# Kernel tuning notes

Measured on AMD Instinct MI355X. Metric: run time of the kernel, lower is better.

The kernel has to match this reference:

```python
import jax, jax.numpy as jnp
import numpy as np

N_NODES = 100000
N_EDGES = 1600000
IN_FEATS = 64
OUT_FEATS = 64
EDGE_FEATS = 1


def setup_inputs() -> dict:
    key = jax.random.key(0)
    ks = jax.random.split(key, 6)
    h = jax.random.normal(ks[0], (N_NODES, IN_FEATS), dtype=jnp.float32)
    e = jax.random.normal(ks[1], (N_EDGES, EDGE_FEATS), dtype=jnp.float32)
    src = jax.random.randint(ks[2], (N_EDGES,), 0, N_NODES, dtype=jnp.int32)
    dst = jax.random.randint(ks[3], (N_EDGES,), 0, N_NODES, dtype=jnp.int32)
    cat_dim = 2 * IN_FEATS + EDGE_FEATS  # 129
    W1 = jax.random.normal(ks[4], (cat_dim, OUT_FEATS), dtype=jnp.float32) / np.sqrt(cat_dim)
    b1 = jnp.zeros((OUT_FEATS,), dtype=jnp.float32)
    W2 = jax.random.normal(ks[5], (OUT_FEATS, OUT_FEATS), dtype=jnp.float32) / np.sqrt(OUT_FEATS)
    b2 = jnp.zeros((OUT_FEATS,), dtype=jnp.float32)
    return {"h": h, "e": e, "src": src, "dst": dst, "W1": W1, "b1": b1, "W2": W2, "b2": b2}


def reference(h, e, src, dst, W1, b1, W2, b2):
    # Gather per-edge features: [src_h | dst_h | e] -> (E, 2*in+edge_dim)
    x = jnp.concatenate([h[src], h[dst], e], axis=1)
    # Two-layer MLP on edges
    m = jax.nn.relu(x @ W1 + b1) @ W2 + b2  # (E, out_feats)
    # Scatter-sum messages to destination nodes
    h_new = jax.ops.segment_sum(m, dst, num_segments=h.shape[0])  # (N, out_feats)
    return h_new
```

## Files before the change

kernel.cpp:

```cpp
#include <hip/hip_runtime.h>
#include <hip/hip_bf16.h>


#define PRE_NPB 128

typedef unsigned int u32;

__device__ __forceinline__ void gload_lds16(const float* g, float* l) {
    __builtin_amdgcn_global_load_lds(
        (const __attribute__((address_space(1))) u32*)g,
        (__attribute__((address_space(3))) u32*)l,
        16, 0, 0);
}

__global__ __launch_bounds__(256) void alloc_offs_kernel(const int* __restrict__ counts,
                                                         int* __restrict__ gcursor,
                                                         int* __restrict__ offs, int n) {
    __shared__ int wsum[4];
    const int i    = blockIdx.x * 256 + threadIdx.x;
    const int lane = threadIdx.x & 63;
    const int wv   = threadIdx.x >> 6;

    const int c = (i < n) ? counts[i] : 0;
    int incl = c;
    #pragma unroll
    for (int d = 1; d < 64; d <<= 1) {
        int v = __shfl_up(incl, d, 64);
        if (lane >= d) incl += v;
    }
    const int excl = incl - c;
    if (lane == 63) wsum[wv] = incl;
    __syncthreads();
    if (threadIdx.x == 0) {
        const int s0 = wsum[0], s1 = wsum[1], s2 = wsum[2], s3 = wsum[3];
        const int b = atomicAdd(gcursor, s0 + s1 + s2 + s3);
        wsum[0] = b; wsum[1] = b + s0; wsum[2] = b + s0 + s1; wsum[3] = b + s0 + s1 + s2;
    }
    __syncthreads();
    if (i < n) offs[i] = wsum[wv] + excl;
}

__global__ void fill_kernel(const int* __restrict__ dst, const int* __restrict__ src,
                            const float* __restrict__ e,
                            const int* __restrict__ offs, const int* __restrict__ rank,
                            int2* __restrict__ meta, int n_edges) {
    const int i = blockIdx.x * blockDim.x + threadIdx.x;
    if (i >= n_edges) return;
    const int d = dst[i];
    meta[offs[d] + rank[i]] = make_int2(src[i], __float_as_int(e[i]));
}

__global__ __launch_bounds__(256, 2) void pre_count_kernel(
    const float* __restrict__ h, const float* __restrict__ W1, const float* __restrict__ b1,
    unsigned short* __restrict__ abf, unsigned short* __restrict__ bsf, int n_nodes,
    const int* __restrict__ dst, int* __restrict__ counts, int* __restrict__ rank,
    int n_edges, int pg)
{
    __shared__ float hbuf[2][64 * 64];
    const int lane = threadIdx.x & 63;
    const int wv   = threadIdx.x >> 6;

    if ((int)blockIdx.x >= pg) {
        const int i = ((int)blockIdx.x - pg) * 256 + threadIdx.x;
        if (i < n_edges) rank[i] = atomicAdd(&counts[dst[i]], 1);
        return;
    }

    const int base = blockIdx.x * PRE_NPB;
    if (base >= n_nodes) return;
    const int nrem   = n_nodes - base;
    const int ntiles = (nrem >= PRE_NPB) ? (PRE_NPB / 64) : ((nrem + 63) >> 6);

    float wreg[128];
    #pragma unroll
    for (int k = 0; k < 128; ++k) wreg[k] = W1[(size_t)k * 64 + lane];
    #pragma unroll
    for (int k = 0; k < 128; ++k) asm volatile("" : "+v"(wreg[k]));
    const float b1l = b1[lane];

    auto stage = [&](int buf, int node_base) {
        if (node_base + 64 <= n_nodes) {
            const float* gsrc = h + (size_t)node_base * 64;
            #pragma unroll
            for (int q = 0; q < 4; ++q) {
                const int c = wv * 4 + q;
                gload_lds16(gsrc + c * 256 + lane * 4, &hbuf[buf][c * 256]);
            }
        } else {
            #pragma unroll
            for (int q = 0; q < 4; ++q) {
                const int f4 = threadIdx.x + 256 * q;
                const long gf = (long)node_base * 16 + f4;
                float4 v = make_float4(0.f, 0.f, 0.f, 0.f);
                if (gf < (long)n_nodes * 16)
                    v = reinterpret_cast<const float4*>(h)[gf];
                reinterpret_cast<float4*>(hbuf[buf])[f4] = v;
            }
        }
    };

    auto consume = [&](int buf, int node_base) {
        for (int i = 0; i < 16; ++i) {
            const int ln = wv * 16 + i;
            const int n  = node_base + ln;
            if (n < n_nodes) {
                const float4* hr = reinterpret_cast<const float4*>(&hbuf[buf][ln * 64]);
                float4 h4[16];
                #pragma unroll
                for (int k4 = 0; k4 < 16; ++k4) h4[k4] = hr[k4];
                float av = 0.f, bv = b1l;
                #pragma unroll
                for (int k4 = 0; k4 < 16; ++k4) {
                    av = fmaf(h4[k4].x, wreg[4 * k4 + 0], av);
                    bv = fmaf(h4[k4].x, wreg[64 + 4 * k4 + 0], bv);
                    av = fmaf(h4[k4].y, wreg[4 * k4 + 1], av);
                    bv = fmaf(h4[k4].y, wreg[64 + 4 * k4 + 1], bv);
                    av = fmaf(h4[k4].z, wreg[4 * k4 + 2], av);
                    bv = fmaf(h4[k4].z, wreg[64 + 4 * k4 + 2], bv);
                    av = fmaf(h4[k4].w, wreg[4 * k4 + 3], av);
                    bv = fmaf(h4[k4].w, wreg[64 + 4 * k4 + 3], bv);
                }
                __hip_bfloat16 ab = __float2bfloat16(av);
                __hip_bfloat16 bb = __float2bfloat16(bv);
                abf[(size_t)n * 64 + lane] = *reinterpret_cast<unsigned short*>(&ab);
                bsf[(size_t)n * 64 + lane] = *reinterpret_cast<unsigned short*>(&bb);
            }
        }
    };

    stage(0, base);
    __syncthreads();
    for (int t = 0; t < ntiles; ++t) {
        if (t + 1 < ntiles) stage((t + 1) & 1, base + (t + 1) * 64);
        consume(t & 1, base + t * 64);
        __syncthreads();
    }
}

__global__ __launch_bounds__(256) void node_accum_kernel(
    const unsigned short* __restrict__ abf, const unsigned short* __restrict__ bsf,
    const float* __restrict__ W1, const float* __restrict__ W2, const float* __restrict__ b2,
    const int* __restrict__ offs, const int* __restrict__ counts,
    const int2* __restrict__ meta, float* __restrict__ out, int n_nodes)
{
    const int lane = threadIdx.x & 63;
    const int wv   = __builtin_amdgcn_readfirstlane(threadIdx.x >> 6);
    const int n    = blockIdx.x * 4 + wv;
    if (n >= n_nodes) return;

    const float basel = __uint_as_float((uint)bsf[(size_t)n * 64 + lane] << 16);
    const float w128l = W1[(size_t)128 * 64 + lane];
    float acc = 0.f;

    const int beg = offs[n];
    const int np  = counts[n];

    for (int c0 = 0; c0 < np; c0 += 64) {
        const int cn = min(np - c0, 64);

        int mx = 0, my = 0;
        if (lane < cn) {
            const int2 m = meta[beg + c0 + lane];
            mx = m.x; my = m.y;
        }

        uint x0=0,x1=0,x2=0,x3=0,x4=0,x5=0,x6=0,x7=0;

        auto ld = [&](int j, uint& x) {
            const int s = __builtin_amdgcn_readlane(mx, j);
            x = (uint)abf[(size_t)s * 64 + lane];
        };
        auto step = [&](int j, uint xr) {
            const float ev = __uint_as_float((uint)__builtin_amdgcn_readlane(my, j));
            const float xv = __uint_as_float(xr << 16);
            acc += fmaxf(fmaf(ev, w128l, basel) + xv, 0.f);
        };

        if (cn > 0) ld(0, x0);
        if (cn > 1) ld(1, x1);
        if (cn > 2) ld(2, x2);
        if (cn > 3) ld(3, x3);
        if (cn > 4) ld(4, x4);
        if (cn > 5) ld(5, x5);
        if (cn > 6) ld(6, x6);
        if (cn > 7) ld(7, x7);

        int i = 0;
        while (i + 16 <= cn) {
            step(i + 0, x0); ld(i + 8,  x0);
            step(i + 1, x1); ld(i + 9,  x1);
            step(i + 2, x2); ld(i + 10, x2);
            step(i + 3, x3); ld(i + 11, x3);
            step(i + 4, x4); ld(i + 12, x4);
            step(i + 5, x5); ld(i + 13, x5);
            step(i + 6, x6); ld(i + 14, x6);
            step(i + 7, x7); ld(i + 15, x7);
            i += 8;
        }
        const int r = cn - i;
        if (r > 0)  { step(i + 0, x0); }  if (r > 8)  { ld(i + 8,  x0); }
        if (r > 1)  { step(i + 1, x1); }  if (r > 9)  { ld(i + 9,  x1); }
        if (r > 2)  { step(i + 2, x2); }  if (r > 10) { ld(i + 10, x2); }
        if (r > 3)  { step(i + 3, x3); }  if (r > 11) { ld(i + 11, x3); }
        if (r > 4)  { step(i + 4, x4); }  if (r > 12) { ld(i + 12, x4); }
        if (r > 5)  { step(i + 5, x5); }  if (r > 13) { ld(i + 13, x5); }
        if (r > 6)  { step(i + 6, x6); }  if (r > 14) { ld(i + 14, x6); }
        if (r > 7)  { step(i + 7, x7); }
        if (r > 8)  { step(i + 8,  x0); }
        if (r > 9)  { step(i + 9,  x1); }
        if (r > 10) { step(i + 10, x2); }
        if (r > 11) { step(i + 11, x3); }
        if (r > 12) { step(i + 12, x4); }
        if (r > 13) { step(i + 13, x5); }
        if (r > 14) { step(i + 14, x6); }
    }

    float o = (float)np * b2[lane];
    #pragma unroll
    for (int j = 0; j < 64; ++j) {
        const float aj = __shfl(acc, j, 64);
        o = fmaf(aj, W2[(size_t)j * 64 + lane], o);
    }
    out[(size_t)n * 64 + lane] = o;
}

extern "C" void kernel_launch(void* const* d_in, const int* in_sizes, int n_in,
                              void* d_out, int out_size, void* d_ws, size_t ws_size,
                              hipStream_t stream) {
    const float* h  = (const float*)d_in[0];
    const float* e  = (const float*)d_in[1];
    const int* src  = (const int*)d_in[2];
    const int* dst  = (const int*)d_in[3];
    const float* W1 = (const float*)d_in[4];
    const float* b1 = (const float*)d_in[5];
    const float* W2 = (const float*)d_in[6];
    const float* b2 = (const float*)d_in[7];
    float* out = (float*)d_out;

    const int n_edges = in_sizes[2];
    const int N = in_sizes[0] / 64;

    int* counts  = (int*)d_ws;
    int* gcursor = counts + N;
    int* offs    = gcursor + 8;
    int* rank    = offs + N;
    int2* meta   = (int2*)(rank + n_edges);
    unsigned short* abf = (unsigned short*)(meta + n_edges);
    unsigned short* bsf = abf + (size_t)64 * N;

    hipMemsetAsync(counts, 0, ((size_t)N + 8) * sizeof(int), stream);

    const int eb = (n_edges + 255) / 256;
    const int nb = (N + 255) / 256;
    const int pg = (N + PRE_NPB - 1) / PRE_NPB;

    pre_count_kernel<<<pg + eb, 256, 0, stream>>>(h, W1, b1, abf, bsf, N,
                                                  dst, counts, rank, n_edges, pg);
    alloc_offs_kernel<<<nb, 256, 0, stream>>>(counts, gcursor, offs, N);
    fill_kernel<<<eb, 256, 0, stream>>>(dst, src, e, offs, rank, meta, n_edges);
    node_accum_kernel<<<(N + 3) / 4, 256, 0, stream>>>(abf, bsf, W1, W2, b2,
                                                       offs, counts, meta, out, N);
}
```

Before: 202.0 us.

## Replace LDS-staged node projection with register-resident h and readlane broadcasts

```diff
diff --git a/kernel.cpp b/kernel.cpp
--- a/kernel.cpp
+++ b/kernel.cpp
@@ -5,13 +5,6 @@
 #define PRE_NPB 128
 
 typedef unsigned int u32;
-
-__device__ __forceinline__ void gload_lds16(const float* g, float* l) {
-    __builtin_amdgcn_global_load_lds(
-        (const __attribute__((address_space(1))) u32*)g,
-        (__attribute__((address_space(3))) u32*)l,
-        16, 0, 0);
-}
 
 __global__ __launch_bounds__(256) void alloc_offs_kernel(const int* __restrict__ counts,
                                                          int* __restrict__ gcursor,
@@ -56,7 +49,6 @@
     const int* __restrict__ dst, int* __restrict__ counts, int* __restrict__ rank,
     int n_edges, int pg)
 {
-    __shared__ float hbuf[2][64 * 64];
     const int lane = threadIdx.x & 63;
     const int wv   = threadIdx.x >> 6;
 
@@ -66,74 +58,88 @@
         return;
     }
 
-    const int base = blockIdx.x * PRE_NPB;
-    if (base >= n_nodes) return;
-    const int nrem   = n_nodes - base;
-    const int ntiles = (nrem >= PRE_NPB) ? (PRE_NPB / 64) : ((nrem + 63) >> 6);
-
-    float wreg[128];
-    #pragma unroll
-    for (int k = 0; k < 128; ++k) wreg[k] = W1[(size_t)k * 64 + lane];
-    #pragma unroll
-    for (int k = 0; k < 128; ++k) asm volatile("" : "+v"(wreg[k]));
-    const float b1l = b1[lane];
-
-    auto stage = [&](int buf, int node_base) {
-        if (node_base + 64 <= n_nodes) {
-            const float* gsrc = h + (size_t)node_base * 64;
+    const int nbase = (blockIdx.x * 4 + wv) * 32;
+    if (nbase >= n_nodes) return;
+
+    const float4* h4p = reinterpret_cast<const float4*>(h);
+
+    auto ldgrp = [&](int g) -> float4 {
+        float4 v = make_float4(0.f, 0.f, 0.f, 0.f);
+        const int row = nbase + 4 * g + (lane >> 4);
+        if (g < 8 && row < n_nodes)
+            v = h4p[(size_t)(nbase + 4 * g) * 16 + lane];
+        return v;
+    };
+
+    {
+        float wreg[64];
+        #pragma unroll
+        for (int k = 0; k < 64; ++k) wreg[k] = W1[(size_t)k * 64 + lane];
+        #pragma unroll
+        for (int k = 0; k < 64; ++k) asm volatile("" : "+v"(wreg[k]));
+
+        float4 cur = ldgrp(0);
+        for (int g = 0; g < 8; ++g) {
+            const float4 nxt = ldgrp(g + 1);
             #pragma unroll
-            for (int q = 0; q < 4; ++q) {
-                const int c = wv * 4 + q;
-                gload_lds16(gsrc + c * 256 + lane * 4, &hbuf[buf][c * 256]);
+            for (int nn = 0; nn < 4; ++nn) {
+                const int n = nbase + 4 * g + nn;
+                if (n < n_nodes) {
+                    float av = 0.f;
+                    #pragma unroll
+                    for (int k4 = 0; k4 < 16; ++k4) {
+                        const int sl = nn * 16 + k4;
+                        const float h0 = __uint_as_float(__builtin_amdgcn_readlane(__float_as_uint(cur.x), sl));
+                        const float h1 = __uint_as_float(__builtin_amdgcn_readlane(__float_as_uint(cur.y), sl));
+                        const float h2 = __uint_as_float(__builtin_amdgcn_readlane(__float_as_uint(cur.z), sl));
+                        const float h3 = __uint_as_float(__builtin_amdgcn_readlane(__float_as_uint(cur.w), sl));
+                        av = fmaf(h0, wreg[4 * k4 + 0], av);
+                        av = fmaf(h1, wreg[4 * k4 + 1], av);
+                        av = fmaf(h2, wreg[4 * k4 + 2], av);
+                        av = fmaf(h3, wreg[4 * k4 + 3], av);
+                    }
+                    __hip_bfloat16 ab = __float2bfloat16(av);
+                    abf[(size_t)n * 64 + lane] = *reinterpret_cast<unsigned short*>(&ab);
+                }
             }
-        } else {
+            cur = nxt;
+        }
+    }
+
+    {
+        float wreg[64];
+        #pragma unroll
+        for (int k = 0; k < 64; ++k) wreg[k] = W1[(size_t)(64 + k) * 64 + lane];
+        #pragma unroll
+        for (int k = 0; k < 64; ++k) asm volatile("" : "+v"(wreg[k]));
+        const float b1l = b1[lane];
+
+        float4 cur = ldgrp(0);
+        for (int g = 0; g < 8; ++g) {
+            const float4 nxt = ldgrp(g + 1);
             #pragma unroll
-            for (int q = 0; q < 4; ++q) {
-                const int f4 = threadIdx.x + 256 * q;
-                const long gf = (long)node_base * 16 + f4;
-                float4 v = make_float4(0.f, 0.f, 0.f, 0.f);
-                if (gf < (long)n_nodes * 16)
-                    v = reinterpret_cast<const float4*>(h)[gf];
-                reinterpret_cast<float4*>(hbuf[buf])[f4] = v;
+            for (int nn = 0; nn < 4; ++nn) {
+                const int n = nbase + 4 * g + nn;
+                if (n < n_nodes) {
+                    float bv = b1l;
+                    #pragma unroll
+                    for (int k4 = 0; k4 < 16; ++k4) {
+                        const int sl = nn * 16 + k4;
+                        const float h0 = __uint_as_float(__builtin_amdgcn_readlane(__float_as_uint(cur.x), sl));
+                        const float h1 = __uint_as_float(__builtin_amdgcn_readlane(__float_as_uint(cur.y), sl));
+                        const float h2 = __uint_as_float(__builtin_amdgcn_readlane(__float_as_uint(cur.z), sl));
+                        const float h3 = __uint_as_float(__builtin_amdgcn_readlane(__float_as_uint(cur.w), sl));
+                        bv = fmaf(h0, wreg[4 * k4 + 0], bv);
+                        bv = fmaf(h1, wreg[4 * k4 + 1], bv);
+                        bv = fmaf(h2, wreg[4 * k4 + 2], bv);
+                        bv = fmaf(h3, wreg[4 * k4 + 3], bv);
+                    }
+                    __hip_bfloat16 bb = __float2bfloat16(bv);
+                    bsf[(size_t)n * 64 + lane] = *reinterpret_cast<unsigned short*>(&bb);
+                }
             }
-        }
-    };
-
-    auto consume = [&](int buf, int node_base) {
-        for (int i = 0; i < 16; ++i) {
-            const int ln = wv * 16 + i;
-            const int n  = node_base + ln;
-            if (n < n_nodes) {
-                const float4* hr = reinterpret_cast<const float4*>(&hbuf[buf][ln * 64]);
-                float4 h4[16];
-                #pragma unroll
-                for (int k4 = 0; k4 < 16; ++k4) h4[k4] = hr[k4];
-                float av = 0.f, bv = b1l;
-                #pragma unroll
-                for (int k4 = 0; k4 < 16; ++k4) {
-                    av = fmaf(h4[k4].x, wreg[4 * k4 + 0], av);
-                    bv = fmaf(h4[k4].x, wreg[64 + 4 * k4 + 0], bv);
-                    av = fmaf(h4[k4].y, wreg[4 * k4 + 1], av);
-                    bv = fmaf(h4[k4].y, wreg[64 + 4 * k4 + 1], bv);
-                    av = fmaf(h4[k4].z, wreg[4 * k4 + 2], av);
-                    bv = fmaf(h4[k4].z, wreg[64 + 4 * k4 + 2], bv);
-                    av = fmaf(h4[k4].w, wreg[4 * k4 + 3], av);
-                    bv = fmaf(h4[k4].w, wreg[64 + 4 * k4 + 3], bv);
-                }
-                __hip_bfloat16 ab = __float2bfloat16(av);
-                __hip_bfloat16 bb = __float2bfloat16(bv);
-                abf[(size_t)n * 64 + lane] = *reinterpret_cast<unsigned short*>(&ab);
-                bsf[(size_t)n * 64 + lane] = *reinterpret_cast<unsigned short*>(&bb);
-            }
-        }
-    };
-
-    stage(0, base);
-    __syncthreads();
-    for (int t = 0; t < ntiles; ++t) {
-        if (t + 1 < ntiles) stage((t + 1) & 1, base + (t + 1) * 64);
-        consume(t & 1, base + t * 64);
-        __syncthreads();
+            cur = nxt;
+        }
     }
 }
 
```

Result: no change. 202.2 us (+0.1%).
